# Kernel optimization log

Measured on AMD Instinct MI355X. Metric: run time of the kernel, lower is better.

Reference implementation:

```python
import jax, jax.numpy as jnp
import numpy as np

B, L, DIM, DFF = 4, 2048, 1024, 4096
EPS = 1e-5

def setup_inputs() -> dict:
    key = jax.random.key(0)
    ks = jax.random.split(key, 10)
    s = 0.02
    return {
        "x": jax.random.normal(ks[0], (B, L, DIM), dtype=jnp.float32),
        "ln_g": jnp.ones((DIM,), jnp.float32),
        "ln_b": jnp.zeros((DIM,), jnp.float32),
        "phazor": jax.random.normal(ks[1], (DIM, 2), dtype=jnp.float32),
        "phazor_init": jax.random.normal(ks[2], (DIM, 2), dtype=jnp.float32),
        "w1": jax.random.normal(ks[3], (DIM, DFF), dtype=jnp.float32) * s,
        "b1": jnp.zeros((DFF,), jnp.float32),
        "w2": jax.random.normal(ks[4], (DFF, DIM), dtype=jnp.float32) * s,
        "b2": jnp.zeros((DIM,), jnp.float32),
        "last_conv_re": jax.random.normal(ks[5], (B, DIM), dtype=jnp.float32),
        "last_conv_im": jax.random.normal(ks[6], (B, DIM), dtype=jnp.float32),
    }

def layer_norm(x, g, b):
    mu = jnp.mean(x, axis=-1, keepdims=True)
    var = jnp.var(x, axis=-1, keepdims=True)
    return (x - mu) * jax.lax.rsqrt(var + EPS) * g + b

def spiral_conv(x, phazor, phazor_init, last_re, last_im):
    # x: [B, L, D] float32
    Lx = x.shape[1]
    p = jax.lax.complex(phazor[:, 0], phazor[:, 1])          # [D]
    p_init = jax.lax.complex(phazor_init[:, 0], phazor_init[:, 1])
    pa = jnp.abs(p)
    p = p / pa * jnp.exp(-pa)                                 # normalized decay phazor
    t = jnp.arange(Lx)
    prog = p[None, :] ** t[:, None]                           # [L, D] p^t
    filt = prog * p_init[None, :]                             # [L, D]
    ffilt = jnp.fft.fft(filt, n=2 * Lx, axis=0)               # [2L, D]
    xf = jnp.fft.fft(x.astype(jnp.complex64), n=2 * Lx, axis=1)  # [B, 2L, D]
    conv = jnp.fft.ifft(ffilt[None] * xf, axis=1)[:, :Lx]     # [B, L, D]
    last = jax.lax.complex(last_re, last_im)                  # [B, D] (detached state)
    conv_with_past = conv + last[:, None, :] * prog[None] * p[None, None, :]
    return conv_with_past.real

def reference(x, ln_g, ln_b, phazor, phazor_init, w1, b1, w2, b2, last_conv_re, last_conv_im):
    x_ = x
    h = layer_norm(x, ln_g, ln_b)
    h = spiral_conv(h, phazor, phazor_init, last_conv_re, last_conv_im)
    x = h + x_
    x_ = x
    h = layer_norm(x, ln_g, ln_b)  # same LayerNorm params reused, as in the source
    h = jax.nn.silu(h @ w1 + b1) @ w2 + b2  # FFN, dropout=0 (eval)
    return h + x_

if __name__ == "__main__":
    out = reference(**setup_inputs())
    print(out.shape, out.dtype)
```

## Files before the change

kernel.cpp:

```cpp
#include <hip/hip_runtime.h>
#include <stdint.h>
#include <stddef.h>

#define DIMC 1024
#define LSEQ 2048
#define BSZ  4
#define DFFC 4096
#define NTOK (BSZ*LSEQ)
#define NCHUNK 32
#define CHUNK 64

typedef __bf16 bf16x8 __attribute__((ext_vector_type(8)));
typedef float  f32x4  __attribute__((ext_vector_type(4)));

__device__ __forceinline__ unsigned short f2bf(float f) {
  unsigned int u = __float_as_uint(f);
  u += 0x7fffu + ((u >> 16) & 1u);
  return (unsigned short)(u >> 16);
}

__device__ __forceinline__ void async16(const void* g, void* l) {
  __builtin_amdgcn_global_load_lds(
      (const __attribute__((address_space(1))) unsigned int*)(uintptr_t)g,
      (__attribute__((address_space(3))) unsigned int*)(uintptr_t)l,
      16, 0, 0);
}

__device__ __forceinline__ void bar() {
  asm volatile("" ::: "memory");
  __builtin_amdgcn_s_barrier();
  asm volatile("" ::: "memory");
}
#define LGKM0 do { asm volatile("s_waitcnt lgkmcnt(0)" ::: "memory"); \
                   __builtin_amdgcn_sched_barrier(0); } while (0)
#define VMCNT(n) asm volatile("s_waitcnt vmcnt(" #n ")" ::: "memory")
template <int N> __device__ __forceinline__ void vmwait() {
  if constexpr (N == 0) VMCNT(0);
  else if constexpr (N == 3) VMCNT(3);
  else if constexpr (N == 4) VMCNT(4);
  else if constexpr (N == 6) VMCNT(6);
  else if constexpr (N == 8) VMCNT(8);
}
#define MFMA_BF16 __builtin_amdgcn_mfma_f32_16x16x32_bf16

__global__ __launch_bounds__(256) void ln_stats(const float* __restrict__ x,
                                                float* __restrict__ mu,
                                                float* __restrict__ rstd) {
  const int token = blockIdx.x;
  const float4* xp = (const float4*)(x + (size_t)token * DIMC);
  float4 v = xp[threadIdx.x];
  float s  = v.x + v.y + v.z + v.w;
  float s2 = v.x*v.x + v.y*v.y + v.z*v.z + v.w*v.w;
  #pragma unroll
  for (int o = 32; o; o >>= 1) { s += __shfl_down(s, o); s2 += __shfl_down(s2, o); }
  __shared__ float sh[8];
  const int lane = threadIdx.x & 63, w = threadIdx.x >> 6;
  if (lane == 0) { sh[w] = s; sh[4 + w] = s2; }
  __syncthreads();
  if (threadIdx.x == 0) {
    float ts  = sh[0] + sh[1] + sh[2] + sh[3];
    float ts2 = sh[4] + sh[5] + sh[6] + sh[7];
    float m = ts * (1.f / DIMC);
    float var = ts2 * (1.f / DIMC) - m * m;
    mu[token] = m;
    rstd[token] = rsqrtf(var + 1e-5f);
  }
}

__global__ __launch_bounds__(256) void ln_fused_bf16(const float* __restrict__ x,
                                                     const float* __restrict__ g,
                                                     const float* __restrict__ bb,
                                                     unsigned short* __restrict__ out) {
  const int token = blockIdx.x;
  const float4* xp = (const float4*)(x + (size_t)token * DIMC);
  float4 v = xp[threadIdx.x];
  float s  = v.x + v.y + v.z + v.w;
  float s2 = v.x*v.x + v.y*v.y + v.z*v.z + v.w*v.w;
  #pragma unroll
  for (int o = 32; o; o >>= 1) { s += __shfl_down(s, o); s2 += __shfl_down(s2, o); }
  __shared__ float sh[10];
  const int lane = threadIdx.x & 63, w = threadIdx.x >> 6;
  if (lane == 0) { sh[w] = s; sh[4 + w] = s2; }
  __syncthreads();
  if (threadIdx.x == 0) {
    float ts  = sh[0] + sh[1] + sh[2] + sh[3];
    float ts2 = sh[4] + sh[5] + sh[6] + sh[7];
    float m = ts * (1.f / DIMC);
    float var = ts2 * (1.f / DIMC) - m * m;
    sh[8] = m;
    sh[9] = rsqrtf(var + 1e-5f);
  }
  __syncthreads();
  const float m = sh[8], r = sh[9];
  float4 gv = ((const float4*)g)[threadIdx.x];
  float4 bv = ((const float4*)bb)[threadIdx.x];
  ushort4 o;
  o.x = f2bf((v.x - m) * r * gv.x + bv.x);
  o.y = f2bf((v.y - m) * r * gv.y + bv.y);
  o.z = f2bf((v.z - m) * r * gv.z + bv.z);
  o.w = f2bf((v.w - m) * r * gv.w + bv.w);
  ((ushort4*)(out + (size_t)token * DIMC))[threadIdx.x] = o;
}

__global__ __launch_bounds__(256) void transpose_bf16(const float* __restrict__ w,
                                                      unsigned short* __restrict__ wt,
                                                      int K, int N) {
  __shared__ float tile[32][33];
  const int n0 = blockIdx.x * 32, k0 = blockIdx.y * 32;
  const int tx = threadIdx.x, ty = threadIdx.y;
  #pragma unroll
  for (int i = 0; i < 32; i += 8)
    tile[ty + i][tx] = w[(size_t)(k0 + ty + i) * N + n0 + tx];
  __syncthreads();
  #pragma unroll
  for (int i = 0; i < 32; i += 8)
    wt[(size_t)(n0 + ty + i) * K + k0 + tx] = f2bf(tile[tx][ty + i]);
}

__device__ __forceinline__ void get_p(const float* __restrict__ phazor, int d,
                                      float& p_re, float& p_im) {
  float pre = phazor[2 * d], pim = phazor[2 * d + 1];
  float a = sqrtf(pre * pre + pim * pim);
  float sc = expf(-a) / a;
  p_re = pre * sc;
  p_im = pim * sc;
}

__global__ __launch_bounds__(256) void scan_phase1(const float* __restrict__ x,
                                                   const float* __restrict__ mu,
                                                   const float* __restrict__ rstd,
                                                   const float* __restrict__ g,
                                                   const float* __restrict__ bb,
                                                   const float* __restrict__ phazor,
                                                   float* __restrict__ Sre,
                                                   float* __restrict__ Sim) {
  const int d = blockIdx.x * 256 + threadIdx.x;
  const int c = blockIdx.y;
  const int b = blockIdx.z;
  float p_re, p_im; get_p(phazor, d, p_re, p_im);
  const float gd = g[d], bd = bb[d];
  const int t0 = c * CHUNK;
  const float* xp  = x + ((size_t)(b * LSEQ + t0)) * DIMC + d;
  const float* mup = mu + b * LSEQ + t0;
  const float* rp  = rstd + b * LSEQ + t0;
  float r_re = 0.f, r_im = 0.f;
  #pragma unroll
  for (int s8 = 0; s8 < CHUNK; s8 += 8) {
    float xv[8];
    #pragma unroll
    for (int k = 0; k < 8; ++k) xv[k] = xp[(size_t)(s8 + k) * DIMC];
    #pragma unroll
    for (int k = 0; k < 8; ++k) {
      float hv = (xv[k] - mup[s8 + k]) * rp[s8 + k] * gd + bd;
      float nr = p_re * r_re - p_im * r_im + hv;
      float ni = p_re * r_im + p_im * r_re;
      r_re = nr; r_im = ni;
    }
  }
  const int bd_i = b * DIMC + d;
  Sre[c * (BSZ * DIMC) + bd_i] = r_re;
  Sim[c * (BSZ * DIMC) + bd_i] = r_im;
}

__global__ __launch_bounds__(256) void scan_phase2(const float* __restrict__ phazor,
                                                   const float* __restrict__ Sre,
                                                   const float* __restrict__ Sim,
                                                   float* __restrict__ Cre,
                                                   float* __restrict__ Cim) {
  const int bd = blockIdx.x * 256 + threadIdx.x;
  const int d = bd & (DIMC - 1);
  float p_re, p_im; get_p(phazor, d, p_re, p_im);
  float br = p_re, bi = p_im;
  #pragma unroll
  for (int i = 0; i < 6; ++i) { float t = br * br - bi * bi; bi = 2.f * br * bi; br = t; }
  float sre[NCHUNK], sim[NCHUNK];
  #pragma unroll
  for (int c = 0; c < NCHUNK; ++c) {
    sre[c] = Sre[c * (BSZ * DIMC) + bd];
    sim[c] = Sim[c * (BSZ * DIMC) + bd];
  }
  float R_re = 0.f, R_im = 0.f;
  #pragma unroll
  for (int c = 0; c < NCHUNK; ++c) {
    Cre[c * (BSZ * DIMC) + bd] = R_re;
    Cim[c * (BSZ * DIMC) + bd] = R_im;
    float nr = br * R_re - bi * R_im + sre[c];
    float ni = br * R_im + bi * R_re + sim[c];
    R_re = nr; R_im = ni;
  }
}

__global__ __launch_bounds__(256) void scan_phase3(const float* __restrict__ x,
                                                   const float* __restrict__ mu,
                                                   const float* __restrict__ rstd,
                                                   const float* __restrict__ g,
                                                   const float* __restrict__ bb,
                                                   const float* __restrict__ phazor,
                                                   const float* __restrict__ phazor_init,
                                                   const float* __restrict__ last_re,
                                                   const float* __restrict__ last_im,
                                                   const float* __restrict__ Cre,
                                                   const float* __restrict__ Cim,
                                                   float* __restrict__ x2) {
  const int d = blockIdx.x * 256 + threadIdx.x;
  const int c = blockIdx.y;
  const int b = blockIdx.z;
  float p_re, p_im; get_p(phazor, d, p_re, p_im);
  const float pi_re = phazor_init[2 * d], pi_im = phazor_init[2 * d + 1];
  const float gd = g[d], bd_ = bb[d];
  const int bd_i = b * DIMC + d;
  float r_re = Cre[c * (BSZ * DIMC) + bd_i];
  float r_im = Cim[c * (BSZ * DIMC) + bd_i];
  float br = p_re, bi = p_im;
  #pragma unroll
  for (int i = 0; i < 6; ++i) { float t = br * br - bi * bi; bi = 2.f * br * bi; br = t; }
  float er = 1.f, ei = 0.f;
  int e = c;
  while (e) {
    if (e & 1) { float t = er * br - ei * bi; ei = er * bi + ei * br; er = t; }
    float t2 = br * br - bi * bi; bi = 2.f * br * bi; br = t2;
    e >>= 1;
  }
  const float lre = last_re[bd_i], lim = last_im[bd_i];
  float q_re = lre * er - lim * ei;
  float q_im = lre * ei + lim * er;
  const int t0 = c * CHUNK;
  const float* xp  = x + ((size_t)(b * LSEQ + t0)) * DIMC + d;
  const float* mup = mu + b * LSEQ + t0;
  const float* rp  = rstd + b * LSEQ + t0;
  float* op = x2 + ((size_t)(b * LSEQ + t0)) * DIMC + d;
  #pragma unroll
  for (int s8 = 0; s8 < CHUNK; s8 += 8) {
    float xv[8];
    #pragma unroll
    for (int k = 0; k < 8; ++k) xv[k] = xp[(size_t)(s8 + k) * DIMC];
    #pragma unroll
    for (int k = 0; k < 8; ++k) {
      float hv = (xv[k] - mup[s8 + k]) * rp[s8 + k] * gd + bd_;
      float nr = p_re * r_re - p_im * r_im + hv;
      float ni = p_re * r_im + p_im * r_re;
      r_re = nr; r_im = ni;
      float nq = p_re * q_re - p_im * q_im;
      q_im = p_re * q_im + p_im * q_re;
      q_re = nq;
      op[(size_t)(s8 + k) * DIMC] = pi_re * r_re - pi_im * r_im + q_re + xv[k];
    }
  }
}

template<int BN, int EPI>
__global__ __launch_bounds__(512, 2) void gemm8(const unsigned short* __restrict__ A,
                                                const unsigned short* __restrict__ Bt,
                                                const float* __restrict__ bias,
                                                const float* __restrict__ resid,
                                                void* __restrict__ outp,
                                                int M, int N, int K) {
  constexpr int AUS = 256 * 32;
  constexpr int BUS = BN * 32;
  constexpr int BUFUS = 2 * AUS + 2 * BUS;
  constexpr int NI = (BN == 256) ? 4 : 2;
  constexpr int LDSUS = (2 * BUFUS > 65536) ? 2 * BUFUS : 65536;
  __shared__ __align__(16) unsigned short lds[LDSUS];

  const int tid  = threadIdx.x;
  const int lane = tid & 63;
  const int wave = tid >> 6;
  const int wm = (wave & 1) * 128;
  const int wn = (wave >> 1) * (BN / 4);
  const int r15 = lane & 15;
  const int cus = ((lane >> 4) ^ ((r15 >> 1) & 3)) * 8;

  int bid = blockIdx.x;
  const int cpx = gridDim.x >> 3;
  bid = (bid & 7) * cpx + (bid >> 3);
  const int ntn = N / BN;
  const int tm = (bid / ntn) * 256;
  const int tn = (bid % ntn) * BN;
  const int NT = K >> 6;

  f32x4 acc[8][NI];
  #pragma unroll
  for (int i = 0; i < 8; ++i)
    #pragma unroll
    for (int j = 0; j < NI; ++j) acc[i][j] = (f32x4){0.f, 0.f, 0.f, 0.f};

  auto stageA1 = [&](int buf, int kk, int k0, int half) {
    unsigned short* blk = lds + buf * BUFUS + kk * AUS;
    const unsigned short* g = A + (size_t)tm * K + k0 + kk * 32;
    const int s = half * 512 + tid;
    const int row = s >> 2;
    const int cg = (s & 3) ^ ((s >> 3) & 3);
    async16(g + (size_t)row * K + cg * 8, blk + (size_t)s * 8);
  };
  auto stageB1 = [&](int buf, int kk, int k0, int half) {
    unsigned short* blk = lds + buf * BUFUS + 2 * AUS + kk * BUS;
    const unsigned short* g = Bt + (size_t)tn * K + k0 + kk * 32;
    const int s = half * 512 + tid;
    const int row = s >> 2;
    const int cg = (s & 3) ^ ((s >> 3) & 3);
    async16(g + (size_t)row * K + cg * 8, blk + (size_t)s * 8);
  };
  auto stageBb = [&](int buf, int kk, int k0) {
    if constexpr (BN == 256) stageB1(buf, kk, k0, 1);
  };
  auto rdA = [&](int buf, int kk, int mi) -> bf16x8 {
    return *(const bf16x8*)(lds + buf * BUFUS + kk * AUS + (wm + mi * 16 + r15) * 32 + cus);
  };
  auto rdB = [&](int buf, int kk, int ni) -> bf16x8 {
    return *(const bf16x8*)(lds + buf * BUFUS + 2 * AUS + kk * BUS + (wn + ni * 16 + r15) * 32 + cus);
  };

  bf16x8 af[4], bq[NI];
  constexpr int VMS = (BN == 256) ? 8 : 6;
  constexpr int VMP = (BN == 256) ? 4 : 3;

#define PH(buf, kk, mh, BREAD, WAIT, ...)                                       \
  {                                                                             \
    _Pragma("unroll")                                                           \
    for (int q = 0; q < 4; ++q) af[q] = rdA(buf, kk, (mh) * 4 + q);             \
    if (BREAD) {                                                                \
      _Pragma("unroll")                                                         \
      for (int n = 0; n < NI; ++n) bq[n] = rdB(buf, kk, n);                     \
    }                                                                           \
    __VA_ARGS__;                                                                \
    bar(); LGKM0;                                                               \
    __builtin_amdgcn_s_setprio(1);                                              \
    _Pragma("unroll")                                                           \
    for (int q = 0; q < 4; ++q)                                                 \
      _Pragma("unroll")                                                         \
      for (int n = 0; n < NI; ++n)                                              \
        acc[(mh) * 4 + q][n] = MFMA_BF16(af[q], bq[n], acc[(mh) * 4 + q][n], 0, 0, 0); \
    __builtin_amdgcn_s_setprio(0);                                              \
    WAIT;                                                                       \
    bar();                                                                      \
  }

  stageA1(0, 0, 0, 0); stageA1(0, 0, 0, 1); stageB1(0, 0, 0, 0); stageBb(0, 0, 0);
  stageA1(0, 1, 0, 0); stageA1(0, 1, 0, 1); stageB1(0, 1, 0, 0); stageBb(0, 1, 0);
  stageA1(1, 0, 64, 0); stageA1(1, 0, 64, 1); stageB1(1, 0, 64, 0); stageBb(1, 0, 64);
  vmwait<VMS>();
  bar();

  for (int i = 0; i < NT / 2 - 1; ++i) {
    const int kb = (2 * i + 1) * 64, kc = kb + 64, kd = kc + 64;
    PH(0, 0, 0, 1, ((void)0),    stageA1(1, 1, kb, 0); stageA1(1, 1, kb, 1))
    PH(0, 0, 1, 0, vmwait<VMS>(), stageB1(1, 1, kb, 0); stageBb(1, 1, kb))
    PH(0, 1, 0, 1, ((void)0),    stageA1(0, 0, kc, 0); stageA1(0, 0, kc, 1))
    PH(0, 1, 1, 0, vmwait<VMS>(), stageB1(0, 0, kc, 0); stageBb(0, 0, kc))
    PH(1, 0, 0, 1, ((void)0),    stageA1(0, 1, kc, 0); stageA1(0, 1, kc, 1))
    PH(1, 0, 1, 0, vmwait<VMS>(), stageB1(0, 1, kc, 0); stageBb(0, 1, kc))
    PH(1, 1, 0, 1, ((void)0),    stageA1(1, 0, kd, 0); stageA1(1, 0, kd, 1))
    PH(1, 1, 1, 0, vmwait<VMS>(), stageB1(1, 0, kd, 0); stageBb(1, 0, kd))
  }

  {
    const int kb = (NT - 1) * 64;
    PH(0, 0, 0, 1, ((void)0),    stageA1(1, 1, kb, 0); stageA1(1, 1, kb, 1))
    PH(0, 0, 1, 0, vmwait<VMS>(), stageB1(1, 1, kb, 0); stageBb(1, 1, kb))
    PH(0, 1, 0, 1, ((void)0),    ((void)0))
    PH(0, 1, 1, 0, vmwait<VMP>(), ((void)0))
    PH(1, 0, 0, 1, ((void)0),    ((void)0))
    PH(1, 0, 1, 0, vmwait<0>(),  ((void)0))
    PH(1, 1, 0, 1, ((void)0),    ((void)0))
    PH(1, 1, 1, 0, ((void)0),    ((void)0))
  }
#undef PH

  const int rg = (lane >> 4) * 4;
  float bias_r[NI];
  #pragma unroll
  for (int ni = 0; ni < NI; ++ni) bias_r[ni] = bias[tn + wn + ni * 16 + r15];

  bar();
  if constexpr (EPI == 0) {
    unsigned short* C = lds;
    #pragma unroll
    for (int mi = 0; mi < 8; ++mi)
      #pragma unroll
      for (int ni = 0; ni < NI; ++ni) {
        const int c0 = wn + ni * 16 + r15;
        #pragma unroll
        for (int j = 0; j < 4; ++j) {
          const int r = wm + mi * 16 + rg + j;
          const int key = (((r & 3) ^ ((r >> 2) & 3)) << 4);
          float v = acc[mi][ni][j] + bias_r[ni];
          v = v / (1.f + __expf(-v));
          C[r * 256 + (c0 ^ key)] = f2bf(v);
        }
      }
    bar();
    #pragma unroll
    for (int i = 0; i < 16; ++i) {
      const int off = i * 4096 + tid * 8;
      const int r = off >> 8;
      const int pc = off & 255;
      const int key = (((r & 3) ^ ((r >> 2) & 3)) << 4);
      bf16x8 v = *(const bf16x8*)(C + off);
      *(bf16x8*)((unsigned short*)outp + (size_t)(tm + r) * N + tn + (pc ^ key)) = v;
    }
  } else {
    float* C = (float*)lds;
    #pragma unroll
    for (int mi = 0; mi < 8; ++mi)
      #pragma unroll
      for (int ni = 0; ni < NI; ++ni) {
        const int c0 = wn + ni * 16 + r15;
        #pragma unroll
        for (int j = 0; j < 4; ++j) {
          const int r = wm + mi * 16 + rg + j;
          const int key = (((r & 3) ^ ((r >> 2) & 3)) << 4);
          C[r * 128 + (c0 ^ key)] = acc[mi][ni][j] + bias_r[ni];
        }
      }
    bar();
    #pragma unroll
    for (int i = 0; i < 16; ++i) {
      const int off = i * 2048 + tid * 4;
      const int r = off >> 7;
      const int pc = off & 127;
      const int key = (((r & 3) ^ ((r >> 2) & 3)) << 4);
      f32x4 v = *(const f32x4*)(C + off);
      const size_t gaddr = (size_t)(tm + r) * N + tn + (pc ^ key);
      f32x4 rv = *(const f32x4*)(resid + gaddr);
      v += rv;
      *(f32x4*)((float*)outp + gaddr) = v;
    }
  }
}

extern "C" void kernel_launch(void* const* d_in, const int* in_sizes, int n_in,
                              void* d_out, int out_size, void* d_ws, size_t ws_size,
                              hipStream_t stream) {
  const float* x           = (const float*)d_in[0];
  const float* ln_g        = (const float*)d_in[1];
  const float* ln_b        = (const float*)d_in[2];
  const float* phazor      = (const float*)d_in[3];
  const float* phazor_init = (const float*)d_in[4];
  const float* w1          = (const float*)d_in[5];
  const float* b1          = (const float*)d_in[6];
  const float* w2          = (const float*)d_in[7];
  const float* b2          = (const float*)d_in[8];
  const float* last_re     = (const float*)d_in[9];
  const float* last_im     = (const float*)d_in[10];
  float* out = (float*)d_out;
  char* ws = (char*)d_ws;
  const size_t MB = 1ull << 20;

  float* x2  = (float*)(ws);
  float* mu1 = (float*)(ws + 32 * MB);
  float* rs1 = (float*)(ws + 32 * MB + 64 * 1024);
  float* Sre = (float*)(ws + 32 * MB + 256 * 1024);
  float* Sim = (float*)(ws + 32 * MB + 768 * 1024);
  float* Cre = (float*)(ws + 32 * MB + 1280 * 1024);
  float* Cim = (float*)(ws + 32 * MB + 1792 * 1024);
  unsigned short* h2  = (unsigned short*)(ws + 35 * MB);
  unsigned short* hid = (unsigned short*)(ws + 51 * MB);
  unsigned short* w1t = (unsigned short*)(ws + 115 * MB);
  unsigned short* w2t = (unsigned short*)(ws + 123 * MB);

  transpose_bf16<<<dim3(DFFC / 32, DIMC / 32), dim3(32, 8), 0, stream>>>(w1, w1t, DIMC, DFFC);
  transpose_bf16<<<dim3(DIMC / 32, DFFC / 32), dim3(32, 8), 0, stream>>>(w2, w2t, DFFC, DIMC);

  ln_stats<<<NTOK, 256, 0, stream>>>(x, mu1, rs1);
  scan_phase1<<<dim3(DIMC / 256, NCHUNK, BSZ), 256, 0, stream>>>(x, mu1, rs1, ln_g, ln_b, phazor, Sre, Sim);
  scan_phase2<<<(BSZ * DIMC) / 256, 256, 0, stream>>>(phazor, Sre, Sim, Cre, Cim);
  scan_phase3<<<dim3(DIMC / 256, NCHUNK, BSZ), 256, 0, stream>>>(x, mu1, rs1, ln_g, ln_b, phazor,
                                                                 phazor_init, last_re, last_im,
                                                                 Cre, Cim, x2);
  ln_fused_bf16<<<NTOK, 256, 0, stream>>>(x2, ln_g, ln_b, h2);

  gemm8<256, 0><<<(NTOK / 256) * (DFFC / 256), 512, 0, stream>>>(h2, w1t, b1, nullptr, hid,
                                                                 NTOK, DFFC, DIMC);
  gemm8<128, 1><<<(NTOK / 256) * (DIMC / 128), 512, 0, stream>>>(hid, w2t, b2, x2, out,
                                                                 NTOK, DIMC, DFFC);
}
```

Measured before the change: 325.4 us.

## Fuse weight transposes with LN stats, fold scan phase2 into phase3, precompute LN2 stats

Merges the two weight transposes and the first LayerNorm statistics into one prep launch. Removes the separate carry-propagation scan kernel: each phase3 block recomputes its own chunk carry by serially combining the preceding chunk sums. Phase3 also accumulates per-token sum and sum-of-squares via wave reductions and atomics, so the second LayerNorm only applies the normalization. This cuts launch count and one full pass over x2, at the cost of redundant carry work in later chunks, atomic contention, and nondeterministic summation order.

```diff
diff --git a/kernel.cpp b/kernel.cpp
--- a/kernel.cpp
+++ b/kernel.cpp
@@ -43,78 +43,53 @@
 }
 #define MFMA_BF16 __builtin_amdgcn_mfma_f32_16x16x32_bf16
 
-__global__ __launch_bounds__(256) void ln_stats(const float* __restrict__ x,
-                                                float* __restrict__ mu,
-                                                float* __restrict__ rstd) {
-  const int token = blockIdx.x;
-  const float4* xp = (const float4*)(x + (size_t)token * DIMC);
-  float4 v = xp[threadIdx.x];
-  float s  = v.x + v.y + v.z + v.w;
-  float s2 = v.x*v.x + v.y*v.y + v.z*v.z + v.w*v.w;
-  #pragma unroll
-  for (int o = 32; o; o >>= 1) { s += __shfl_down(s, o); s2 += __shfl_down(s2, o); }
+__global__ __launch_bounds__(256) void prep(const float* __restrict__ w1,
+                                            const float* __restrict__ w2,
+                                            unsigned short* __restrict__ w1t,
+                                            unsigned short* __restrict__ w2t,
+                                            const float* __restrict__ x,
+                                            float* __restrict__ mu,
+                                            float* __restrict__ rstd,
+                                            float* __restrict__ tokstat) {
+  __shared__ float tile[32][33];
   __shared__ float sh[8];
-  const int lane = threadIdx.x & 63, w = threadIdx.x >> 6;
-  if (lane == 0) { sh[w] = s; sh[4 + w] = s2; }
-  __syncthreads();
-  if (threadIdx.x == 0) {
-    float ts  = sh[0] + sh[1] + sh[2] + sh[3];
-    float ts2 = sh[4] + sh[5] + sh[6] + sh[7];
-    float m = ts * (1.f / DIMC);
-    float var = ts2 * (1.f / DIMC) - m * m;
-    mu[token] = m;
-    rstd[token] = rsqrtf(var + 1e-5f);
-  }
-}
-
-__global__ __launch_bounds__(256) void ln_fused_bf16(const float* __restrict__ x,
-                                                     const float* __restrict__ g,
-                                                     const float* __restrict__ bb,
-                                                     unsigned short* __restrict__ out) {
-  const int token = blockIdx.x;
-  const float4* xp = (const float4*)(x + (size_t)token * DIMC);
-  float4 v = xp[threadIdx.x];
-  float s  = v.x + v.y + v.z + v.w;
-  float s2 = v.x*v.x + v.y*v.y + v.z*v.z + v.w*v.w;
-  #pragma unroll
-  for (int o = 32; o; o >>= 1) { s += __shfl_down(s, o); s2 += __shfl_down(s2, o); }
-  __shared__ float sh[10];
-  const int lane = threadIdx.x & 63, w = threadIdx.x >> 6;
-  if (lane == 0) { sh[w] = s; sh[4 + w] = s2; }
-  __syncthreads();
-  if (threadIdx.x == 0) {
-    float ts  = sh[0] + sh[1] + sh[2] + sh[3];
-    float ts2 = sh[4] + sh[5] + sh[6] + sh[7];
-    float m = ts * (1.f / DIMC);
-    float var = ts2 * (1.f / DIMC) - m * m;
-    sh[8] = m;
-    sh[9] = rsqrtf(var + 1e-5f);
-  }
-  __syncthreads();
-  const float m = sh[8], r = sh[9];
-  float4 gv = ((const float4*)g)[threadIdx.x];
-  float4 bv = ((const float4*)bb)[threadIdx.x];
-  ushort4 o;
-  o.x = f2bf((v.x - m) * r * gv.x + bv.x);
-  o.y = f2bf((v.y - m) * r * gv.y + bv.y);
-  o.z = f2bf((v.z - m) * r * gv.z + bv.z);
-  o.w = f2bf((v.w - m) * r * gv.w + bv.w);
-  ((ushort4*)(out + (size_t)token * DIMC))[threadIdx.x] = o;
-}
-
-__global__ __launch_bounds__(256) void transpose_bf16(const float* __restrict__ w,
-                                                      unsigned short* __restrict__ wt,
-                                                      int K, int N) {
-  __shared__ float tile[32][33];
-  const int n0 = blockIdx.x * 32, k0 = blockIdx.y * 32;
-  const int tx = threadIdx.x, ty = threadIdx.y;
-  #pragma unroll
-  for (int i = 0; i < 32; i += 8)
-    tile[ty + i][tx] = w[(size_t)(k0 + ty + i) * N + n0 + tx];
-  __syncthreads();
-  #pragma unroll
-  for (int i = 0; i < 32; i += 8)
-    wt[(size_t)(n0 + ty + i) * K + k0 + tx] = f2bf(tile[tx][ty + i]);
+  const int blk = blockIdx.x;
+  if (blk < 8192) {
+    const float* w; unsigned short* wt; int K, N, bi;
+    if (blk < 4096) { w = w1; wt = w1t; K = DIMC; N = DFFC; bi = blk; }
+    else            { w = w2; wt = w2t; K = DFFC; N = DIMC; bi = blk - 4096; }
+    const int nbx = N / 32;
+    const int n0 = (bi % nbx) * 32, k0 = (bi / nbx) * 32;
+    const int tx = threadIdx.x & 31, ty = threadIdx.x >> 5;
+    #pragma unroll
+    for (int i = 0; i < 32; i += 8)
+      tile[ty + i][tx] = w[(size_t)(k0 + ty + i) * N + n0 + tx];
+    __syncthreads();
+    #pragma unroll
+    for (int i = 0; i < 32; i += 8)
+      wt[(size_t)(n0 + ty + i) * K + k0 + tx] = f2bf(tile[tx][ty + i]);
+  } else {
+    const int token = blk - 8192;
+    const float4* xp = (const float4*)(x + (size_t)token * DIMC);
+    float4 v = xp[threadIdx.x];
+    float s  = v.x + v.y + v.z + v.w;
+    float s2 = v.x*v.x + v.y*v.y + v.z*v.z + v.w*v.w;
+    #pragma unroll
+    for (int o = 32; o; o >>= 1) { s += __shfl_down(s, o); s2 += __shfl_down(s2, o); }
+    const int lane = threadIdx.x & 63, w = threadIdx.x >> 6;
+    if (lane == 0) { sh[w] = s; sh[4 + w] = s2; }
+    __syncthreads();
+    if (threadIdx.x == 0) {
+      float ts  = sh[0] + sh[1] + sh[2] + sh[3];
+      float ts2 = sh[4] + sh[5] + sh[6] + sh[7];
+      float m = ts * (1.f / DIMC);
+      float var = ts2 * (1.f / DIMC) - m * m;
+      mu[token] = m;
+      rstd[token] = rsqrtf(var + 1e-5f);
+      tokstat[2 * token] = 0.f;
+      tokstat[2 * token + 1] = 0.f;
+    }
+  }
 }
 
 __device__ __forceinline__ void get_p(const float* __restrict__ phazor, int d,
@@ -162,34 +137,6 @@
   Sim[c * (BSZ * DIMC) + bd_i] = r_im;
 }
 
-__global__ __launch_bounds__(256) void scan_phase2(const float* __restrict__ phazor,
-                                                   const float* __restrict__ Sre,
-                                                   const float* __restrict__ Sim,
-                                                   float* __restrict__ Cre,
-                                                   float* __restrict__ Cim) {
-  const int bd = blockIdx.x * 256 + threadIdx.x;
-  const int d = bd & (DIMC - 1);
-  float p_re, p_im; get_p(phazor, d, p_re, p_im);
-  float br = p_re, bi = p_im;
-  #pragma unroll
-  for (int i = 0; i < 6; ++i) { float t = br * br - bi * bi; bi = 2.f * br * bi; br = t; }
-  float sre[NCHUNK], sim[NCHUNK];
-  #pragma unroll
-  for (int c = 0; c < NCHUNK; ++c) {
-    sre[c] = Sre[c * (BSZ * DIMC) + bd];
-    sim[c] = Sim[c * (BSZ * DIMC) + bd];
-  }
-  float R_re = 0.f, R_im = 0.f;
-  #pragma unroll
-  for (int c = 0; c < NCHUNK; ++c) {
-    Cre[c * (BSZ * DIMC) + bd] = R_re;
-    Cim[c * (BSZ * DIMC) + bd] = R_im;
-    float nr = br * R_re - bi * R_im + sre[c];
-    float ni = br * R_im + bi * R_re + sim[c];
-    R_re = nr; R_im = ni;
-  }
-}
-
 __global__ __launch_bounds__(256) void scan_phase3(const float* __restrict__ x,
                                                    const float* __restrict__ mu,
                                                    const float* __restrict__ rstd,
@@ -199,27 +146,45 @@
                                                    const float* __restrict__ phazor_init,
                                                    const float* __restrict__ last_re,
                                                    const float* __restrict__ last_im,
-                                                   const float* __restrict__ Cre,
-                                                   const float* __restrict__ Cim,
-                                                   float* __restrict__ x2) {
+                                                   const float* __restrict__ Sre,
+                                                   const float* __restrict__ Sim,
+                                                   float* __restrict__ x2,
+                                                   float* __restrict__ tokstat) {
+  __shared__ float shs[CHUNK][4], shs2[CHUNK][4];
   const int d = blockIdx.x * 256 + threadIdx.x;
   const int c = blockIdx.y;
   const int b = blockIdx.z;
+  const int lane = threadIdx.x & 63, wv = threadIdx.x >> 6;
   float p_re, p_im; get_p(phazor, d, p_re, p_im);
   const float pi_re = phazor_init[2 * d], pi_im = phazor_init[2 * d + 1];
   const float gd = g[d], bd_ = bb[d];
   const int bd_i = b * DIMC + d;
-  float r_re = Cre[c * (BSZ * DIMC) + bd_i];
-  float r_im = Cim[c * (BSZ * DIMC) + bd_i];
   float br = p_re, bi = p_im;
   #pragma unroll
   for (int i = 0; i < 6; ++i) { float t = br * br - bi * bi; bi = 2.f * br * bi; br = t; }
+  float r_re = 0.f, r_im = 0.f;
+  for (int j0 = 0; j0 < c; j0 += 8) {
+    float sr[8], si[8];
+    const int jn = (c - j0 < 8) ? (c - j0) : 8;
+    for (int k = 0; k < jn; ++k) {
+      sr[k] = Sre[(j0 + k) * (BSZ * DIMC) + bd_i];
+      si[k] = Sim[(j0 + k) * (BSZ * DIMC) + bd_i];
+    }
+    for (int k = 0; k < jn; ++k) {
+      float nr = br * r_re - bi * r_im + sr[k];
+      float ni = br * r_im + bi * r_re + si[k];
+      r_re = nr; r_im = ni;
+    }
+  }
   float er = 1.f, ei = 0.f;
-  int e = c;
-  while (e) {
-    if (e & 1) { float t = er * br - ei * bi; ei = er * bi + ei * br; er = t; }
-    float t2 = br * br - bi * bi; bi = 2.f * br * bi; br = t2;
-    e >>= 1;
+  {
+    float qr = br, qi = bi;
+    int e = c;
+    while (e) {
+      if (e & 1) { float t = er * qr - ei * qi; ei = er * qi + ei * qr; er = t; }
+      float t2 = qr * qr - qi * qi; qi = 2.f * qr * qi; qr = t2;
+      e >>= 1;
+    }
   }
   const float lre = last_re[bd_i], lim = last_im[bd_i];
   float q_re = lre * er - lim * ei;
@@ -243,9 +208,44 @@
       float nq = p_re * q_re - p_im * q_im;
       q_im = p_re * q_im + p_im * q_re;
       q_re = nq;
-      op[(size_t)(s8 + k) * DIMC] = pi_re * r_re - pi_im * r_im + q_re + xv[k];
-    }
-  }
+      float opv = pi_re * r_re - pi_im * r_im + q_re + xv[k];
+      op[(size_t)(s8 + k) * DIMC] = opv;
+      float a1 = opv, a2 = opv * opv;
+      #pragma unroll
+      for (int o = 32; o; o >>= 1) { a1 += __shfl_xor(a1, o); a2 += __shfl_xor(a2, o); }
+      if (lane == 0) { shs[s8 + k][wv] = a1; shs2[s8 + k][wv] = a2; }
+    }
+  }
+  __syncthreads();
+  if (threadIdx.x < CHUNK) {
+    const int s = threadIdx.x;
+    float s1 = shs[s][0] + shs[s][1] + shs[s][2] + shs[s][3];
+    float s2 = shs2[s][0] + shs2[s][1] + shs2[s][2] + shs2[s][3];
+    const int tok = b * LSEQ + t0 + s;
+    atomicAdd(&tokstat[2 * tok], s1);
+    atomicAdd(&tokstat[2 * tok + 1], s2);
+  }
+}
+
+__global__ __launch_bounds__(256) void ln_apply(const float* __restrict__ x2,
+                                                const float* __restrict__ tokstat,
+                                                const float* __restrict__ g,
+                                                const float* __restrict__ bb,
+                                                unsigned short* __restrict__ out) {
+  const int token = blockIdx.x;
+  const float s1 = tokstat[2 * token], s2 = tokstat[2 * token + 1];
+  const float m = s1 * (1.f / DIMC);
+  const float var = s2 * (1.f / DIMC) - m * m;
+  const float r = rsqrtf(var + 1e-5f);
+  float4 v = ((const float4*)(x2 + (size_t)token * DIMC))[threadIdx.x];
+  float4 gv = ((const float4*)g)[threadIdx.x];
+  float4 bv = ((const float4*)bb)[threadIdx.x];
+  ushort4 o;
+  o.x = f2bf((v.x - m) * r * gv.x + bv.x);
+  o.y = f2bf((v.y - m) * r * gv.y + bv.y);
+  o.z = f2bf((v.z - m) * r * gv.z + bv.z);
+  o.w = f2bf((v.w - m) * r * gv.w + bv.w);
+  ((ushort4*)(out + (size_t)token * DIMC))[threadIdx.x] = o;
 }
 
 template<int BN, int EPI>
@@ -451,23 +451,19 @@
   float* rs1 = (float*)(ws + 32 * MB + 64 * 1024);
   float* Sre = (float*)(ws + 32 * MB + 256 * 1024);
   float* Sim = (float*)(ws + 32 * MB + 768 * 1024);
-  float* Cre = (float*)(ws + 32 * MB + 1280 * 1024);
-  float* Cim = (float*)(ws + 32 * MB + 1792 * 1024);
+  float* tokstat = (float*)(ws + 32 * MB + 1280 * 1024);
   unsigned short* h2  = (unsigned short*)(ws + 35 * MB);
   unsigned short* hid = (unsigned short*)(ws + 51 * MB);
   unsigned short* w1t = (unsigned short*)(ws + 115 * MB);
   unsigned short* w2t = (unsigned short*)(ws + 123 * MB);
 
-  transpose_bf16<<<dim3(DFFC / 32, DIMC / 32), dim3(32, 8), 0, stream>>>(w1, w1t, DIMC, DFFC);
-  transpose_bf16<<<dim3(DIMC / 32, DFFC / 32), dim3(32, 8), 0, stream>>>(w2, w2t, DFFC, DIMC);
-
-  ln_stats<<<NTOK, 256, 0, stream>>>(x, mu1, rs1);
-  scan_phase1<<<dim3(DIMC / 256, NCHUNK, BSZ), 256, 0, stream>>>(x, mu1, rs1, ln_g, ln_b, phazor, Sre, Sim);
-  scan_phase2<<<(BSZ * DIMC) / 256, 256, 0, stream>>>(phazor, Sre, Sim, Cre, Cim);
+  prep<<<16384, 256, 0, stream>>>(w1, w2, w1t, w2t, x, mu1, rs1, tokstat);
+  scan_phase1<<<dim3(DIMC / 256, NCHUNK, BSZ), 256, 0, stream>>>(x, mu1, rs1, ln_g, ln_b,
+                                                                 phazor, Sre, Sim);
   scan_phase3<<<dim3(DIMC / 256, NCHUNK, BSZ), 256, 0, stream>>>(x, mu1, rs1, ln_g, ln_b, phazor,
                                                                  phazor_init, last_re, last_im,
-                                                                 Cre, Cim, x2);
-  ln_fused_bf16<<<NTOK, 256, 0, stream>>>(x2, ln_g, ln_b, h2);
+                                                                 Sre, Sim, x2, tokstat);
+  ln_apply<<<NTOK, 256, 0, stream>>>(x2, tokstat, ln_g, ln_b, h2);
 
   gemm8<256, 0><<<(NTOK / 256) * (DFFC / 256), 512, 0, stream>>>(h2, w1t, b1, nullptr, hid,
                                                                  NTOK, DFFC, DIMC);
```

Result: slower. 349.8 us (+7.5%).
